# Optimization experiments

Measured on AMD Instinct MI355X. Metric: run time of the kernel, lower is better.

The kernel has to match this reference:

```python
import jax, jax.numpy as jnp
import numpy as np

B, T, E, H, V = 256, 32, 512, 512, 3000
SKIP = 2


def setup_inputs() -> dict:
    key = jax.random.key(0)
    ks = jax.random.split(key, 12)
    # sorted-descending ragged lengths, max forced to T (pack_padded_sequence requires descending)
    lengths = np.sort(np.asarray(jax.random.randint(ks[0], (B,), T // 2, T + 1)))[::-1].copy()
    lengths[0] = T
    s = 0.05
    return {
        "image_features": jax.random.normal(ks[1], (B, E // 2), jnp.float32),
        "text_features": jax.random.normal(ks[2], (B, E // 2), jnp.float32),
        "h0": jnp.zeros((B, H), jnp.float32),
        "c0": jnp.zeros((B, H), jnp.float32),
        "embed_table": jax.random.normal(ks[3], (V, E), jnp.float32) * 0.02,
        "W_ih": jax.random.normal(ks[4], (4 * H, E), jnp.float32) * s,
        "W_hh": jax.random.normal(ks[5], (4 * H, H), jnp.float32) * s,
        "b_ih": jnp.zeros((4 * H,), jnp.float32),
        "b_hh": jnp.zeros((4 * H,), jnp.float32),
        "W_out": jax.random.normal(ks[6], (V, 2 * H), jnp.float32) * s,
        "b_out": jnp.zeros((V,), jnp.float32),
        "answer": jax.random.randint(ks[7], (B, T), 0, V),
        "answer_lengths": lengths,  # numpy int array (static)
    }


def _lstm_cell(x, hx, cx, W_ih, W_hh, b_ih, b_hh):
    # torch.nn.LSTMCell math: gates ordered i, f, g, o
    g = x @ W_ih.T + b_ih + hx @ W_hh.T + b_hh
    i, f, gg, o = jnp.split(g, 4, axis=-1)
    cy = jax.nn.sigmoid(f) * cx + jax.nn.sigmoid(i) * jnp.tanh(gg)
    hy = jax.nn.sigmoid(o) * jnp.tanh(cy)
    return hy, cy


def _packed_indices(lengths, max_len, batch):
    # torch pack_padded_sequence (batch_first) ordering: for each timestep t,
    # rows 0..batch_sizes[t] of the (descending-sorted) batch, time-major concat.
    lengths = np.asarray(lengths)
    idx = np.concatenate([t * batch + np.arange(int((lengths > t).sum())) for t in range(max_len)])
    return jnp.asarray(idx)


def reference(image_features, text_features, h0, c0, embed_table,
              W_ih, W_hh, b_ih, b_hh, W_out, b_out, answer, answer_lengths):
    batch = image_features.shape[0]
    max_len = int(np.max(np.asarray(answer_lengths)))
    combined = jnp.concatenate([image_features, text_features], axis=1)  # [B, E]
    emb = embed_table[answer]                                            # [B, T, E]
    # inputs over time: step 0 = combined, steps 1..max_len-1 = embedded answer tokens
    xs = jnp.concatenate([combined[:, None, :], emb[:, : max_len - 1, :]], axis=1)
    xs = jnp.transpose(xs, (1, 0, 2))                                    # [T, B, E]
    ts = jnp.arange(max_len)

    def step(carry, inp):
        hx, cx, h_m2, h_m1, c_m2, c_m1 = carry
        t, x = inp
        hy, cy = _lstm_cell(x, hx, cx, W_ih, W_hh, b_ih, b_hh)
        # periodic skip-state residual: applied to the carried state AFTER storing hy/cy
        cond = (t >= SKIP) & (t % (SKIP + 1) == 0)
        hx_n = jnp.where(cond, hy + h_m2, hy)
        cx_n = jnp.where(cond, cy + c_m2, cy)
        return (hx_n, cx_n, h_m1, hy, c_m1, cy), (hy, cy)

    z = jnp.zeros_like(h0)
    (_, _, _, _, _, _), (hs, cs) = jax.lax.scan(step, (h0, c0, z, z, z, z), (ts, xs))
    results = jnp.concatenate([hs, cs], axis=-1)          # [T, B, 2H], time-major
    flat = results.reshape(max_len * batch, 2 * results.shape[-1] // 2)
    idx = _packed_indices(answer_lengths, max_len, batch)
    packed = flat[idx]                                    # [sum(lengths), 2H]
    return packed @ W_out.T + b_out                       # [sum(lengths), V]
```

## Files before the change

### kernel.cpp

```cpp
#include <hip/hip_runtime.h>
#include <hip/hip_bf16.h>

#define T_STEPS 32
#define BATCH 256
#define EDIM 512
#define HDIM 512
#define G4 2048
#define VOCAB 3000
#define VPAD 3072

typedef short bf16x8 __attribute__((ext_vector_type(8)));
typedef float f32x4 __attribute__((ext_vector_type(4)));

__device__ __forceinline__ unsigned short f2b(float f){
  union { float f; unsigned int u; } x; x.f = f;
  unsigned int u = x.u;
  unsigned int r = (u + 0x7fffu + ((u >> 16) & 1u)) >> 16;
  return (unsigned short)r;
}
__device__ __forceinline__ float b2f(unsigned short h){
  union { unsigned int u; float f; } x; x.u = ((unsigned int)h) << 16;
  return x.f;
}
__device__ __forceinline__ float sigm(float x){ return 1.0f / (1.0f + expf(-x)); }

__device__ __forceinline__ void gload_lds16(const unsigned short* g, unsigned short* l){
  __builtin_amdgcn_global_load_lds(
      (const __attribute__((address_space(1))) unsigned int*)g,
      (__attribute__((address_space(3))) unsigned int*)l, 16, 0, 0);
}


__global__ void k_cvt_w(const float* __restrict__ wih, const float* __restrict__ whh,
                        unsigned short* __restrict__ o_ih, unsigned short* __restrict__ o_hh){
  int i = blockIdx.x * blockDim.x + threadIdx.x;
  int n1 = G4 * EDIM;
  if (i < n1) o_ih[i] = f2b(wih[i]);
  else { int j = i - n1; if (j < G4 * HDIM) o_hh[j] = f2b(whh[j]); }
}

__global__ void k_cvt_wout(const float* __restrict__ in, unsigned short* __restrict__ out){
  int i = blockIdx.x * blockDim.x + threadIdx.x;
  if (i >= VPAD * 1024) return;
  int r = i >> 10, c = i & 1023;
  float v = (r < VOCAB) ? in[r * 1024 + c] : 0.0f;
  out[i] = f2b(v);
}

__global__ void k_build_xs(const float* __restrict__ img, const float* __restrict__ txt,
                           const float* __restrict__ emb, const int* __restrict__ ans,
                           unsigned short* __restrict__ xs){
  int i = blockIdx.x * blockDim.x + threadIdx.x;
  if (i >= T_STEPS * BATCH * EDIM) return;
  int e = i & (EDIM - 1);
  int r = i >> 9;
  int t = r >> 8, b = r & 255;
  float v;
  if (t == 0) v = (e < 256) ? img[b * 256 + e] : txt[b * 256 + (e - 256)];
  else { int tok = ans[b * T_STEPS + (t - 1)]; v = emb[(size_t)tok * EDIM + e]; }
  xs[i] = f2b(v);
}

__global__ void k_init_carry(const float* __restrict__ h0, const float* __restrict__ c0,
                             unsigned short* __restrict__ hx, float* __restrict__ cx){
  int i = blockIdx.x * blockDim.x + threadIdx.x;
  if (i < BATCH * HDIM){ hx[i] = f2b(h0[i]); cx[i] = c0[i]; }
}

__global__ void k_lens(const int* __restrict__ lengths, int* __restrict__ bs,
                       int* __restrict__ roff, int* __restrict__ meta,
                       int* __restrict__ rmap){
  __shared__ int s[T_STEPS];
  __shared__ int sroff[T_STEPS + 1];
  int t = threadIdx.x;
  if (t < T_STEPS){
    int c = 0;
    for (int i = 0; i < BATCH; i++) c += (lengths[i] > t) ? 1 : 0;
    s[t] = c; bs[t] = c;
  }
  __syncthreads();
  if (t == 0){
    int acc = 0;
    for (int u = 0; u < T_STEPS; u++){ sroff[u] = acc; roff[u] = acc; acc += s[u]; }
    sroff[T_STEPS] = acc;
    meta[0] = acc;
  }
  __syncthreads();
  int ntot = sroff[T_STEPS];
  for (int r = t; r < T_STEPS * BATCH; r += 64){
    int tt = r >> 8, b = r & 255;
    if (b < s[tt]) rmap[sroff[tt] + b] = r;
  }
  for (int r = ntot + t; r < T_STEPS * BATCH; r += 64) rmap[r] = -1;
}

template<int K>
__device__ __forceinline__ void gemm_tile(const unsigned short* __restrict__ A,
                                          const unsigned short* __restrict__ B,
                                          int row0, int col0,
                                          unsigned short* As, unsigned short* Bs,
                                          f32x4 acc[4][4]){
  const int tid = threadIdx.x, w = tid >> 6, l = tid & 63;
  const int la = l & 15, lkq = l >> 4;
  const int sr = l >> 3;
  const int ss = (l & 7) ^ sr;
  const int wr = (w >> 1) * 64, wc = (w & 1) * 64;
  const unsigned short* gA = A + (size_t)(row0 + w * 32 + sr) * K + ss * 8;
  const unsigned short* gB = B + (size_t)(col0 + w * 32 + sr) * K + ss * 8;
  unsigned short* lA = As + (w * 32) * 64;
  unsigned short* lB = Bs + (w * 32) * 64;
  for (int k0 = 0; k0 < K; k0 += 64){
#pragma unroll
    for (int i = 0; i < 4; i++){
      gload_lds16(gA + (size_t)i * 8 * K + k0, lA + i * 8 * 64);
      gload_lds16(gB + (size_t)i * 8 * K + k0, lB + i * 8 * 64);
    }
    __syncthreads();
#pragma unroll
    for (int kk = 0; kk < 2; kk++){
      bf16x8 a[4], b[4];
#pragma unroll
      for (int i = 0; i < 4; i++){
        int r = wr + i * 16 + la;
        a[i] = *(const bf16x8*)(As + r * 64 + (((kk * 4 + lkq) ^ (r & 7)) << 3));
      }
#pragma unroll
      for (int i = 0; i < 4; i++){
        int r = wc + i * 16 + la;
        b[i] = *(const bf16x8*)(Bs + r * 64 + (((kk * 4 + lkq) ^ (r & 7)) << 3));
      }
#pragma unroll
      for (int mi = 0; mi < 4; mi++)
#pragma unroll
        for (int ni = 0; ni < 4; ni++)
          acc[mi][ni] = __builtin_amdgcn_mfma_f32_16x16x32_bf16(a[mi], b[ni], acc[mi][ni], 0, 0, 0);
    }
    __syncthreads();
  }
}

__global__ __launch_bounds__(256) void k_gemm_xw(const unsigned short* __restrict__ A,
                                                 const unsigned short* __restrict__ W,
                                                 const float* __restrict__ bih,
                                                 const float* __restrict__ bhh,
                                                 unsigned short* __restrict__ C){
  __shared__ unsigned short As[128 * 64], Bs[128 * 64];
  int row0 = blockIdx.x * 128, col0 = blockIdx.y * 128;
  f32x4 acc[4][4] = {};
  gemm_tile<EDIM>(A, W, row0, col0, As, Bs, acc);
  int tid = threadIdx.x, w = tid >> 6, l = tid & 63;
  int la = l & 15, r4 = (l >> 4) * 4;
  int wr = (w >> 1) * 64, wc = (w & 1) * 64;
#pragma unroll
  for (int ni = 0; ni < 4; ni++){
    int col = col0 + wc + ni * 16 + la;
    float bias = bih[col] + bhh[col];
#pragma unroll
    for (int mi = 0; mi < 4; mi++)
#pragma unroll
      for (int j = 0; j < 4; j++){
        int row = row0 + wr + mi * 16 + r4 + j;
        C[(size_t)row * G4 + col] = f2b(acc[mi][ni][j] + bias);
      }
  }
}

__global__ __launch_bounds__(256, 2) void k_lstm_step(
    const unsigned short* __restrict__ XWt,
    const unsigned short* __restrict__ Whh,
    const unsigned short* __restrict__ hin,
    unsigned short* __restrict__ hout,
    float* __restrict__ cxio,
    unsigned short* __restrict__ hs_t,
    unsigned short* __restrict__ cs_t,
    const unsigned short* __restrict__ hs_m2,
    const unsigned short* __restrict__ cs_m2,
    int do_res){
  __shared__ unsigned short hA[16 * 512];
  __shared__ float gbuf[4][16][17];
  const int w = threadIdx.x >> 6, l = threadIdx.x & 63;
  const int la = l & 15, lkq = l >> 4;
  const int row0 = blockIdx.x * 16;
  const int hc0  = blockIdx.y * 16;
#pragma unroll
  for (int i = 0; i < 4; i++){
    int r = i * 4 + w;
    gload_lds16(hin + (size_t)(row0 + r) * HDIM + ((l ^ (r & 7)) << 3), hA + r * 512);
  }
  const unsigned short* Bp = Whh + (size_t)(w * HDIM + hc0 + la) * HDIM + lkq * 8;
  bf16x8 b[16];
#pragma unroll
  for (int kk = 0; kk < 16; kk++) b[kk] = *(const bf16x8*)(Bp + kk * 32);
  const int r4 = lkq * 4;
  float x[4];
#pragma unroll
  for (int j = 0; j < 4; j++)
    x[j] = b2f(XWt[(size_t)(row0 + r4 + j) * G4 + w * HDIM + hc0 + la]);
  __syncthreads();
  f32x4 acc = {};
#pragma unroll
  for (int kk = 0; kk < 16; kk++){
    bf16x8 a = *(const bf16x8*)(hA + la * 512 + (((kk * 4 + lkq) ^ (la & 7)) << 3));
    acc = __builtin_amdgcn_mfma_f32_16x16x32_bf16(a, b[kk], acc, 0, 0, 0);
  }
#pragma unroll
  for (int j = 0; j < 4; j++) gbuf[w][r4 + j][la] = acc[j] + x[j];
  __syncthreads();
  {
    int r = threadIdx.x >> 4, c = threadIdx.x & 15;
    size_t p = (size_t)(row0 + r) * HDIM + hc0 + c;
    float gi = gbuf[0][r][c], gf = gbuf[1][r][c], gg = gbuf[2][r][c], go = gbuf[3][r][c];
    float cprev = cxio[p];
    float cy = sigm(gf) * cprev + sigm(gi) * tanhf(gg);
    float hy = sigm(go) * tanhf(cy);
    hs_t[p] = f2b(hy);
    cs_t[p] = f2b(cy);
    float hn = hy, cn = cy;
    if (do_res){ hn += b2f(hs_m2[p]); cn += b2f(cs_m2[p]); }
    hout[p] = f2b(hn);
    cxio[p] = cn;
  }
}

__global__ __launch_bounds__(256) void k_gemm_out(const unsigned short* __restrict__ hs,
                                                  const unsigned short* __restrict__ cs,
                                                  const unsigned short* __restrict__ Wo,
                                                  const float* __restrict__ bout,
                                                  const int* __restrict__ meta,
                                                  const int* __restrict__ rmap,
                                                  float* __restrict__ out){
  int ntot = meta[0];
  int row0 = blockIdx.x * 128, col0 = blockIdx.y * 128;
  if (row0 >= ntot) return;
  __shared__ unsigned short As[128 * 64], Bs[128 * 64];
  const int tid = threadIdx.x, w = tid >> 6, l = tid & 63;
  const int la = l & 15, lkq = l >> 4;
  const int sr = l >> 3, ss = (l & 7) ^ sr;
  const int wr = (w >> 1) * 64, wc = (w & 1) * 64;
  int srow[4];
#pragma unroll
  for (int i = 0; i < 4; i++){
    int rr = rmap[row0 + w * 32 + sr + i * 8];
    srow[i] = rr < 0 ? 0 : rr;
  }
  const unsigned short* gB = Wo + (size_t)(col0 + w * 32 + sr) * 1024 + ss * 8;
  unsigned short* lA = As + (w * 32) * 64;
  unsigned short* lB = Bs + (w * 32) * 64;
  f32x4 acc[4][4] = {};
  for (int k0 = 0; k0 < 1024; k0 += 64){
#pragma unroll
    for (int i = 0; i < 4; i++){
      const unsigned short* srcA = (k0 < 512)
          ? hs + (size_t)srow[i] * 512 + k0 + ss * 8
          : cs + (size_t)srow[i] * 512 + (k0 - 512) + ss * 8;
      gload_lds16(srcA, lA + i * 8 * 64);
      gload_lds16(gB + (size_t)i * 8 * 1024 + k0, lB + i * 8 * 64);
    }
    __syncthreads();
#pragma unroll
    for (int kk = 0; kk < 2; kk++){
      bf16x8 a[4], b[4];
#pragma unroll
      for (int i = 0; i < 4; i++){
        int r = wr + i * 16 + la;
        a[i] = *(const bf16x8*)(As + r * 64 + (((kk * 4 + lkq) ^ (r & 7)) << 3));
      }
#pragma unroll
      for (int i = 0; i < 4; i++){
        int r = wc + i * 16 + la;
        b[i] = *(const bf16x8*)(Bs + r * 64 + (((kk * 4 + lkq) ^ (r & 7)) << 3));
      }
#pragma unroll
      for (int mi = 0; mi < 4; mi++)
#pragma unroll
        for (int ni = 0; ni < 4; ni++)
          acc[mi][ni] = __builtin_amdgcn_mfma_f32_16x16x32_bf16(a[mi], b[ni], acc[mi][ni], 0, 0, 0);
    }
    __syncthreads();
  }
  int r4 = (l >> 4) * 4;
#pragma unroll
  for (int ni = 0; ni < 4; ni++){
    int col = col0 + wc + ni * 16 + la;
    if (col >= VOCAB) continue;
    float bias = bout[col];
#pragma unroll
    for (int mi = 0; mi < 4; mi++)
#pragma unroll
      for (int j = 0; j < 4; j++){
        int row = row0 + wr + mi * 16 + r4 + j;
        if (row < ntot) out[(size_t)row * VOCAB + col] = acc[mi][ni][j] + bias;
      }
  }
}

extern "C" void kernel_launch(void* const* d_in, const int* in_sizes, int n_in,
                              void* d_out, int out_size, void* d_ws, size_t ws_size,
                              hipStream_t stream){
  const float* img   = (const float*)d_in[0];
  const float* txt   = (const float*)d_in[1];
  const float* h0    = (const float*)d_in[2];
  const float* c0    = (const float*)d_in[3];
  const float* emb   = (const float*)d_in[4];
  const float* W_ih  = (const float*)d_in[5];
  const float* W_hh  = (const float*)d_in[6];
  const float* b_ih  = (const float*)d_in[7];
  const float* b_hh  = (const float*)d_in[8];
  const float* W_out = (const float*)d_in[9];
  const float* b_out = (const float*)d_in[10];
  const int* answer  = (const int*)d_in[11];
  const int* lengths = (const int*)d_in[12];
  float* out = (float*)d_out;

  char* ws = (char*)d_ws;
  size_t off = 0;
  auto alloc = [&](size_t bytes) -> void* {
    void* p = ws + off; off += (bytes + 255) & ~(size_t)255; return p;
  };
  unsigned short* Wih_b = (unsigned short*)alloc((size_t)G4 * EDIM * 2);
  unsigned short* Whh_b = (unsigned short*)alloc((size_t)G4 * HDIM * 2);
  unsigned short* Wo_b  = (unsigned short*)alloc((size_t)VPAD * 1024 * 2);
  unsigned short* xs    = (unsigned short*)alloc((size_t)T_STEPS * BATCH * EDIM * 2);
  unsigned short* XW    = (unsigned short*)alloc((size_t)T_STEPS * BATCH * G4 * 2);
  unsigned short* hs    = (unsigned short*)alloc((size_t)T_STEPS * BATCH * HDIM * 2);
  unsigned short* cs    = (unsigned short*)alloc((size_t)T_STEPS * BATCH * HDIM * 2);
  unsigned short* hxA   = (unsigned short*)alloc((size_t)BATCH * HDIM * 2);
  unsigned short* hxB   = (unsigned short*)alloc((size_t)BATCH * HDIM * 2);
  float* cx             = (float*)alloc((size_t)BATCH * HDIM * 4);
  int* bsz  = (int*)alloc(T_STEPS * 4);
  int* roff = (int*)alloc(T_STEPS * 4);
  int* meta = (int*)alloc(256);
  int* rmap = (int*)alloc(T_STEPS * BATCH * 4);

  k_cvt_w<<<(2 * G4 * EDIM + 255) / 256, 256, 0, stream>>>(W_ih, W_hh, Wih_b, Whh_b);
  k_cvt_wout<<<(VPAD * 1024 + 255) / 256, 256, 0, stream>>>(W_out, Wo_b);
  k_build_xs<<<(T_STEPS * BATCH * EDIM + 255) / 256, 256, 0, stream>>>(img, txt, emb, answer, xs);
  k_init_carry<<<(BATCH * HDIM + 255) / 256, 256, 0, stream>>>(h0, c0, hxA, cx);
  k_lens<<<1, 64, 0, stream>>>(lengths, bsz, roff, meta, rmap);

  k_gemm_xw<<<dim3(T_STEPS * BATCH / 128, G4 / 128), 256, 0, stream>>>(xs, Wih_b, b_ih, b_hh, XW);

  unsigned short* hbuf[2] = { hxA, hxB };
  for (int t = 0; t < T_STEPS; t++){
    int do_res = (t >= 2 && (t % 3) == 0) ? 1 : 0;
    int tm2 = (t >= 2) ? (t - 2) : 0;
    k_lstm_step<<<dim3(BATCH / 16, HDIM / 16), 256, 0, stream>>>(
        XW + (size_t)t * BATCH * G4, Whh_b, hbuf[t & 1], hbuf[(t + 1) & 1], cx,
        hs + (size_t)t * BATCH * HDIM, cs + (size_t)t * BATCH * HDIM,
        hs + (size_t)tm2 * BATCH * HDIM, cs + (size_t)tm2 * BATCH * HDIM, do_res);
  }

  k_gemm_out<<<dim3(T_STEPS * BATCH / 128, VPAD / 128), 256, 0, stream>>>(hs, cs, Wo_b, b_out, meta, rmap, out);
}
```

Measured before the change: 355.4 us.

## Double-buffer LDS tiles in input and output GEMMs to overlap loads with MFMA

Both the input-projection GEMM and the output GEMM now use two LDS buffers and prefetch the next K-tile with direct-to-LDS loads while MFMAs run on the current one. Explicit vmcnt waits, s_barrier and sched_barrier fences replace the per-tile __syncthreads. The aim is to hide global-load latency behind compute, at the cost of twice the LDS per block, which may lower occupancy. The recurrent LSTM step kernel is unchanged and probably dominates total time.

```diff
diff --git a/kernel.cpp b/kernel.cpp
--- a/kernel.cpp
+++ b/kernel.cpp
@@ -94,63 +94,71 @@
   for (int r = ntot + t; r < T_STEPS * BATCH; r += 64) rmap[r] = -1;
 }
 
-template<int K>
-__device__ __forceinline__ void gemm_tile(const unsigned short* __restrict__ A,
-                                          const unsigned short* __restrict__ B,
-                                          int row0, int col0,
-                                          unsigned short* As, unsigned short* Bs,
-                                          f32x4 acc[4][4]){
-  const int tid = threadIdx.x, w = tid >> 6, l = tid & 63;
-  const int la = l & 15, lkq = l >> 4;
-  const int sr = l >> 3;
-  const int ss = (l & 7) ^ sr;
-  const int wr = (w >> 1) * 64, wc = (w & 1) * 64;
-  const unsigned short* gA = A + (size_t)(row0 + w * 32 + sr) * K + ss * 8;
-  const unsigned short* gB = B + (size_t)(col0 + w * 32 + sr) * K + ss * 8;
-  unsigned short* lA = As + (w * 32) * 64;
-  unsigned short* lB = Bs + (w * 32) * 64;
-  for (int k0 = 0; k0 < K; k0 += 64){
-#pragma unroll
-    for (int i = 0; i < 4; i++){
-      gload_lds16(gA + (size_t)i * 8 * K + k0, lA + i * 8 * 64);
-      gload_lds16(gB + (size_t)i * 8 * K + k0, lB + i * 8 * 64);
-    }
-    __syncthreads();
-#pragma unroll
-    for (int kk = 0; kk < 2; kk++){
-      bf16x8 a[4], b[4];
-#pragma unroll
-      for (int i = 0; i < 4; i++){
-        int r = wr + i * 16 + la;
-        a[i] = *(const bf16x8*)(As + r * 64 + (((kk * 4 + lkq) ^ (r & 7)) << 3));
-      }
-#pragma unroll
-      for (int i = 0; i < 4; i++){
-        int r = wc + i * 16 + la;
-        b[i] = *(const bf16x8*)(Bs + r * 64 + (((kk * 4 + lkq) ^ (r & 7)) << 3));
-      }
-#pragma unroll
-      for (int mi = 0; mi < 4; mi++)
-#pragma unroll
-        for (int ni = 0; ni < 4; ni++)
-          acc[mi][ni] = __builtin_amdgcn_mfma_f32_16x16x32_bf16(a[mi], b[ni], acc[mi][ni], 0, 0, 0);
-    }
-    __syncthreads();
-  }
-}
+
+#define GEMM_COMPUTE(BUFA, BUFB)                                                     \
+  {                                                                                  \
+    _Pragma("unroll")                                                                \
+    for (int kk = 0; kk < 2; kk++){                                                  \
+      bf16x8 a[4], b[4];                                                             \
+      _Pragma("unroll")                                                              \
+      for (int i = 0; i < 4; i++){                                                   \
+        int r = wr + i * 16 + la;                                                    \
+        a[i] = *(const bf16x8*)((BUFA) + r * 64 + (((kk * 4 + lkq) ^ (r & 7)) << 3));\
+      }                                                                              \
+      _Pragma("unroll")                                                              \
+      for (int i = 0; i < 4; i++){                                                   \
+        int r = wc + i * 16 + la;                                                    \
+        b[i] = *(const bf16x8*)((BUFB) + r * 64 + (((kk * 4 + lkq) ^ (r & 7)) << 3));\
+      }                                                                              \
+      _Pragma("unroll")                                                              \
+      for (int mi = 0; mi < 4; mi++)                                                 \
+        _Pragma("unroll")                                                            \
+        for (int ni = 0; ni < 4; ni++)                                               \
+          acc[mi][ni] = __builtin_amdgcn_mfma_f32_16x16x32_bf16(a[mi], b[ni], acc[mi][ni], 0, 0, 0); \
+    }                                                                                \
+  }
+
+#define SB0 __builtin_amdgcn_sched_barrier(0)
 
 __global__ __launch_bounds__(256) void k_gemm_xw(const unsigned short* __restrict__ A,
                                                  const unsigned short* __restrict__ W,
                                                  const float* __restrict__ bih,
                                                  const float* __restrict__ bhh,
                                                  unsigned short* __restrict__ C){
-  __shared__ unsigned short As[128 * 64], Bs[128 * 64];
-  int row0 = blockIdx.x * 128, col0 = blockIdx.y * 128;
+  __shared__ unsigned short As[2][128 * 64], Bs[2][128 * 64];
+  const int K = EDIM, NT = EDIM / 64;
+  const int tid = threadIdx.x, w = tid >> 6, l = tid & 63;
+  const int la = l & 15, lkq = l >> 4;
+  const int sr = l >> 3, ss = (l & 7) ^ sr;
+  const int wr = (w >> 1) * 64, wc = (w & 1) * 64;
+  const int row0 = blockIdx.x * 128, col0 = blockIdx.y * 128;
+  const unsigned short* gA = A + (size_t)(row0 + w * 32 + sr) * K + ss * 8;
+  const unsigned short* gB = W + (size_t)(col0 + w * 32 + sr) * K + ss * 8;
   f32x4 acc[4][4] = {};
-  gemm_tile<EDIM>(A, W, row0, col0, As, Bs, acc);
-  int tid = threadIdx.x, w = tid >> 6, l = tid & 63;
-  int la = l & 15, r4 = (l >> 4) * 4;
-  int wr = (w >> 1) * 64, wc = (w & 1) * 64;
+
+#define STAGE_XW(BUF, K0)                                                          \
+  { _Pragma("unroll")                                                              \
+    for (int i = 0; i < 4; i++){                                                   \
+      gload_lds16(gA + (size_t)i * 8 * K + (K0), As[BUF] + (w * 32 + i * 8) * 64); \
+      gload_lds16(gB + (size_t)i * 8 * K + (K0), Bs[BUF] + (w * 32 + i * 8) * 64); \
+    } }
+
+  STAGE_XW(0, 0);
+  asm volatile("s_waitcnt vmcnt(0)" ::: "memory"); SB0;
+  __builtin_amdgcn_s_barrier(); SB0;
+  for (int kt = 0; kt < NT; ++kt){
+    int cur = kt & 1;
+    if (kt + 1 < NT){
+      STAGE_XW(cur ^ 1, (kt + 1) * 64); SB0;
+      asm volatile("s_waitcnt vmcnt(8)" ::: "memory");
+    } else {
+      asm volatile("s_waitcnt vmcnt(0)" ::: "memory");
+    }
+    SB0; __builtin_amdgcn_s_barrier(); SB0;
+    GEMM_COMPUTE(As[cur], Bs[cur]);
+    SB0; __builtin_amdgcn_s_barrier(); SB0;
+  }
+  int r4 = (l >> 4) * 4;
 #pragma unroll
   for (int ni = 0; ni < 4; ni++){
     int col = col0 + wc + ni * 16 + la;
@@ -232,7 +240,8 @@
   int ntot = meta[0];
   int row0 = blockIdx.x * 128, col0 = blockIdx.y * 128;
   if (row0 >= ntot) return;
-  __shared__ unsigned short As[128 * 64], Bs[128 * 64];
+  __shared__ unsigned short As[2][128 * 64], Bs[2][128 * 64];
+  const int NT = 1024 / 64;
   const int tid = threadIdx.x, w = tid >> 6, l = tid & 63;
   const int la = l & 15, lkq = l >> 4;
   const int sr = l >> 3, ss = (l & 7) ^ sr;
@@ -244,39 +253,33 @@
     srow[i] = rr < 0 ? 0 : rr;
   }
   const unsigned short* gB = Wo + (size_t)(col0 + w * 32 + sr) * 1024 + ss * 8;
-  unsigned short* lA = As + (w * 32) * 64;
-  unsigned short* lB = Bs + (w * 32) * 64;
   f32x4 acc[4][4] = {};
-  for (int k0 = 0; k0 < 1024; k0 += 64){
-#pragma unroll
-    for (int i = 0; i < 4; i++){
-      const unsigned short* srcA = (k0 < 512)
-          ? hs + (size_t)srow[i] * 512 + k0 + ss * 8
-          : cs + (size_t)srow[i] * 512 + (k0 - 512) + ss * 8;
-      gload_lds16(srcA, lA + i * 8 * 64);
-      gload_lds16(gB + (size_t)i * 8 * 1024 + k0, lB + i * 8 * 64);
+
+#define STAGE_OUT(BUF, K0)                                                          \
+  { _Pragma("unroll")                                                               \
+    for (int i = 0; i < 4; i++){                                                    \
+      const unsigned short* srcA = ((K0) < 512)                                     \
+          ? hs + (size_t)srow[i] * 512 + (K0) + ss * 8                              \
+          : cs + (size_t)srow[i] * 512 + ((K0) - 512) + ss * 8;                     \
+      gload_lds16(srcA, As[BUF] + (w * 32 + i * 8) * 64);                           \
+      gload_lds16(gB + (size_t)i * 8 * 1024 + (K0), Bs[BUF] + (w * 32 + i * 8) * 64);\
+    } }
+
+  STAGE_OUT(0, 0);
+  asm volatile("s_waitcnt vmcnt(0)" ::: "memory"); SB0;
+  __builtin_amdgcn_s_barrier(); SB0;
+  for (int kt = 0; kt < NT; ++kt){
+    int cur = kt & 1;
+    if (kt + 1 < NT){
+      int k0n = (kt + 1) * 64;
+      STAGE_OUT(cur ^ 1, k0n); SB0;
+      asm volatile("s_waitcnt vmcnt(8)" ::: "memory");
+    } else {
+      asm volatile("s_waitcnt vmcnt(0)" ::: "memory");
     }
-    __syncthreads();
-#pragma unroll
-    for (int kk = 0; kk < 2; kk++){
-      bf16x8 a[4], b[4];
-#pragma unroll
-      for (int i = 0; i < 4; i++){
-        int r = wr + i * 16 + la;
-        a[i] = *(const bf16x8*)(As + r * 64 + (((kk * 4 + lkq) ^ (r & 7)) << 3));
-      }
-#pragma unroll
-      for (int i = 0; i < 4; i++){
-        int r = wc + i * 16 + la;
-        b[i] = *(const bf16x8*)(Bs + r * 64 + (((kk * 4 + lkq) ^ (r & 7)) << 3));
-      }
-#pragma unroll
-      for (int mi = 0; mi < 4; mi++)
-#pragma unroll
-        for (int ni = 0; ni < 4; ni++)
-          acc[mi][ni] = __builtin_amdgcn_mfma_f32_16x16x32_bf16(a[mi], b[ni], acc[mi][ni], 0, 0, 0);
-    }
-    __syncthreads();
+    SB0; __builtin_amdgcn_s_barrier(); SB0;
+    GEMM_COMPUTE(As[cur], Bs[cur]);
+    SB0; __builtin_amdgcn_s_barrier(); SB0;
   }
   int r4 = (l >> 4) * 4;
 #pragma unroll
```

Measured after the change: 358.2 us. Within noise of the previous version (+0.8%).
